# Performance work log

Measured on AMD Instinct MI355X. Metric: run time of the kernel, lower is better.

The kernel has to match this reference:

```python
import jax, jax.numpy as jnp
import numpy as np

N, M, D = 8192, 8192, 256

def setup_inputs() -> dict:
    key = jax.random.key(0)
    k1, k2, k3, k4 = jax.random.split(key, 4)
    x1 = jax.random.normal(k1, (N, D), dtype=jnp.float32)
    x2 = jax.random.normal(k2, (M, D), dtype=jnp.float32)
    alpha_raw = jax.random.normal(k3, (D,), dtype=jnp.float32)      # nn.Parameter(torch.randn(input_dim))
    variance_raw = jnp.ones((1,), dtype=jnp.float32)                # nn.Parameter(torch.ones(1))
    return {"x1": x1, "x2": x2, "alpha_raw": alpha_raw, "variance_raw": variance_raw}

def reference(x1, x2, alpha_raw, variance_raw):
    # alpha = softmax(alpha_raw^2), variance = variance_raw^2
    alpha = jax.nn.softmax(alpha_raw ** 2)                          # (D,)
    variance = variance_raw ** 2                                    # (1,)
    # GEMM rewrite of sum_d alpha_d (x1_i - x2_j)^2:
    #   ||x1*sqrt(a)||^2 - 2 (x1*sqrt(a))(x2*sqrt(a))^T + ||x2*sqrt(a)||^2
    sa = jnp.sqrt(alpha)
    a = x1 * sa                                                     # (N, D)
    b = x2 * sa                                                     # (M, D)
    sq = (jnp.sum(a * a, axis=-1)[:, None]
          - 2.0 * (a @ b.T)
          + jnp.sum(b * b, axis=-1)[None, :])                       # (N, M)
    sq = jnp.maximum(sq, 0.0)  # numerical guard; exact value is non-negative
    kernel = variance * jnp.exp(-0.5 * sq)                          # (N, M)
    if kernel.shape[0] == 1:
        kernel = jnp.squeeze(kernel)
    return kernel
```

## Files before the change

kernel.cpp:

```cpp
#include <hip/hip_runtime.h>
#include <stdint.h>

#define NROWS 8192
#define MCOLS 8192
#define KDIM  256

typedef __bf16 bf16x8 __attribute__((ext_vector_type(8)));
typedef float  floatx4 __attribute__((ext_vector_type(4)));

__device__ __forceinline__ unsigned short f32_to_bf16_rne(float f) {
    unsigned int u = __float_as_uint(f);
    u += 0x7FFFu + ((u >> 16) & 1u);
    return (unsigned short)(u >> 16);
}
__device__ __forceinline__ float bf16_to_f32(unsigned short h) {
    return __uint_as_float(((unsigned int)h) << 16);
}

__device__ __forceinline__ void async16(const void* g, void* l) {
    __builtin_amdgcn_global_load_lds(
        (const __attribute__((address_space(1))) unsigned int*)g,
        (__attribute__((address_space(3))) unsigned int*)l,
        16, 0, 0);
}

__global__ void prep_alpha(const float* __restrict__ araw, float* __restrict__ sa) {
    __shared__ float buf[256];
    int d = threadIdx.x;
    float z = araw[d];
    z = z * z;
    buf[d] = z;
    __syncthreads();
    for (int s = 128; s > 0; s >>= 1) {
        if (d < s) buf[d] = fmaxf(buf[d], buf[d + s]);
        __syncthreads();
    }
    float mx = buf[0];
    __syncthreads();
    float e = __expf(z - mx);
    buf[d] = e;
    __syncthreads();
    for (int s = 128; s > 0; s >>= 1) {
        if (d < s) buf[d] += buf[d + s];
        __syncthreads();
    }
    float sum = buf[0];
    sa[d] = sqrtf(e / sum);
}

__global__ void prep_rows(const float* __restrict__ x, const float* __restrict__ sa,
                          unsigned short* __restrict__ mat, float* __restrict__ rnorm) {
    __shared__ float buf[256];
    int row = blockIdx.x;
    int d = threadIdx.x;
    float v = x[(size_t)row * KDIM + d] * sa[d];
    unsigned short h = f32_to_bf16_rne(v);
    mat[(size_t)row * KDIM + d] = h;
    float fv = bf16_to_f32(h);
    buf[d] = fv * fv;
    __syncthreads();
    for (int s = 128; s > 0; s >>= 1) {
        if (d < s) buf[d] += buf[d + s];
        __syncthreads();
    }
    if (d == 0) rnorm[row] = buf[0];
}

__global__ __launch_bounds__(256) void rbf_gemm(
    const unsigned short* __restrict__ A, const unsigned short* __restrict__ B,
    const float* __restrict__ ra, const float* __restrict__ rb,
    const float* __restrict__ vraw, float* __restrict__ out)
{
    __shared__ unsigned short As[128 * 64];
    __shared__ unsigned short Bs[128 * 64];

    const int tid  = threadIdx.x;
    const int lane = tid & 63;
    const int wave = tid >> 6;
    const int bm = blockIdx.y;
    const int bn = blockIdx.x;
    const int wm = (wave & 1) * 64;
    const int wn = (wave >> 1) * 64;
    const int quad = lane >> 4;
    const int l15  = lane & 15;

    floatx4 acc[4][4];
#pragma unroll
    for (int i = 0; i < 4; i++)
#pragma unroll
        for (int j = 0; j < 4; j++) acc[i][j] = (floatx4)0.0f;

    for (int k0 = 0; k0 < KDIM; k0 += 64) {
#pragma unroll
        for (int it = 0; it < 4; ++it) {
            int c   = it * 256 + tid;
            int row = c >> 3;
            int kc  = c & 7;
            int gkc = kc ^ (row & 7);
            const unsigned short* gA = A + (size_t)(bm * 128 + row) * KDIM + k0 + gkc * 8;
            const unsigned short* gB = B + (size_t)(bn * 128 + row) * KDIM + k0 + gkc * 8;
            async16(gA, &As[c * 8]);
            async16(gB, &Bs[c * 8]);
        }
        __syncthreads();

#pragma unroll
        for (int ks = 0; ks < 2; ++ks) {
            bf16x8 af[4], bfr[4];
            int kc = ks * 4 + quad;
#pragma unroll
            for (int t = 0; t < 4; ++t) {
                int m  = wm + t * 16 + l15;
                int sa_ = m * 8 + (kc ^ (m & 7));
                af[t]  = *(const bf16x8*)&As[sa_ * 8];
                int n  = wn + t * 16 + l15;
                int sb_ = n * 8 + (kc ^ (n & 7));
                bfr[t] = *(const bf16x8*)&Bs[sb_ * 8];
            }
#pragma unroll
            for (int ti = 0; ti < 4; ++ti)
#pragma unroll
                for (int tj = 0; tj < 4; ++tj)
                    acc[ti][tj] = __builtin_amdgcn_mfma_f32_16x16x32_bf16(
                        af[ti], bfr[tj], acc[ti][tj], 0, 0, 0);
        }
        __syncthreads();
    }

    float variance = vraw[0] * vraw[0];
    float rbv[4];
#pragma unroll
    for (int tj = 0; tj < 4; ++tj) rbv[tj] = rb[bn * 128 + wn + tj * 16 + l15];
#pragma unroll
    for (int ti = 0; ti < 4; ++ti) {
        int rowbase = bm * 128 + wm + ti * 16 + quad * 4;
        float rav[4];
#pragma unroll
        for (int r = 0; r < 4; ++r) rav[r] = ra[rowbase + r];
#pragma unroll
        for (int tj = 0; tj < 4; ++tj) {
            int col = bn * 128 + wn + tj * 16 + l15;
#pragma unroll
            for (int r = 0; r < 4; ++r) {
                float s = rav[r] + rbv[tj] - 2.0f * acc[ti][tj][r];
                s = fmaxf(s, 0.0f);
                out[(size_t)(rowbase + r) * MCOLS + col] = variance * __expf(-0.5f * s);
            }
        }
    }
}

extern "C" void kernel_launch(void* const* d_in, const int* in_sizes, int n_in,
                              void* d_out, int out_size, void* d_ws, size_t ws_size,
                              hipStream_t stream) {
    const float* x1   = (const float*)d_in[0];
    const float* x2   = (const float*)d_in[1];
    const float* araw = (const float*)d_in[2];
    const float* vraw = (const float*)d_in[3];
    float* out = (float*)d_out;

    char* ws = (char*)d_ws;
    float* sa = (float*)ws;
    float* ra = (float*)(ws + 1024);
    float* rb = (float*)(ws + 1024 + 32768);
    unsigned short* Amat = (unsigned short*)(ws + 66560);
    unsigned short* Bmat = (unsigned short*)(ws + 66560 + (size_t)NROWS * KDIM * 2);

    prep_alpha<<<1, 256, 0, stream>>>(araw, sa);
    prep_rows<<<NROWS, 256, 0, stream>>>(x1, sa, Amat, ra);
    prep_rows<<<MCOLS, 256, 0, stream>>>(x2, sa, Bmat, rb);

    dim3 grid(MCOLS / 128, NROWS / 128);
    rbf_gemm<<<grid, 256, 0, stream>>>(Amat, Bmat, ra, rb, vraw, out);
}
```

Before: 311.1 us.

## Vectorize output stores via transposed MFMA, merge row prep, swizzle block order

Swaps the MFMA operand order so each lane holds four consecutive output columns. The epilogue can then write float4 nontemporal stores instead of scalar strided stores, with the distance algebra folded to -0.5 scaling and a fminf. The two row-prep launches are merged into one wave-per-row kernel that uses vector loads and a shuffle reduction, removing the shared-memory tree. GEMM blocks are remapped into groups of 8 row tiles for better L2 reuse of the A and B tiles.

```diff
diff --git a/kernel.cpp b/kernel.cpp
--- a/kernel.cpp
+++ b/kernel.cpp
@@ -48,22 +48,37 @@
     sa[d] = sqrtf(e / sum);
 }
 
-__global__ void prep_rows(const float* __restrict__ x, const float* __restrict__ sa,
-                          unsigned short* __restrict__ mat, float* __restrict__ rnorm) {
-    __shared__ float buf[256];
-    int row = blockIdx.x;
-    int d = threadIdx.x;
-    float v = x[(size_t)row * KDIM + d] * sa[d];
-    unsigned short h = f32_to_bf16_rne(v);
-    mat[(size_t)row * KDIM + d] = h;
-    float fv = bf16_to_f32(h);
-    buf[d] = fv * fv;
-    __syncthreads();
-    for (int s = 128; s > 0; s >>= 1) {
-        if (d < s) buf[d] += buf[d + s];
-        __syncthreads();
-    }
-    if (d == 0) rnorm[row] = buf[0];
+__global__ __launch_bounds__(256) void prep_rows_all(
+    const float* __restrict__ x1, const float* __restrict__ x2,
+    const float* __restrict__ sa,
+    unsigned short* __restrict__ Amat, unsigned short* __restrict__ Bmat,
+    float* __restrict__ ra, float* __restrict__ rb)
+{
+    int rg   = blockIdx.x * 4 + (threadIdx.x >> 6);
+    int lane = threadIdx.x & 63;
+
+    const float* x; unsigned short* mat; float* rn; int row;
+    if (rg < NROWS) { x = x1; mat = Amat; rn = ra; row = rg; }
+    else            { x = x2; mat = Bmat; rn = rb; row = rg - NROWS; }
+
+    float4 sv = ((const float4*)sa)[lane];
+    float4 xv = ((const float4*)(x + (size_t)row * KDIM))[lane];
+
+    unsigned short h0 = f32_to_bf16_rne(xv.x * sv.x);
+    unsigned short h1 = f32_to_bf16_rne(xv.y * sv.y);
+    unsigned short h2 = f32_to_bf16_rne(xv.z * sv.z);
+    unsigned short h3 = f32_to_bf16_rne(xv.w * sv.w);
+
+    ushort4 hv; hv.x = h0; hv.y = h1; hv.z = h2; hv.w = h3;
+    ((ushort4*)(mat + (size_t)row * KDIM))[lane] = hv;
+
+    float f0 = bf16_to_f32(h0), f1 = bf16_to_f32(h1),
+          f2 = bf16_to_f32(h2), f3 = bf16_to_f32(h3);
+    float nrm = f0 * f0 + f1 * f1 + f2 * f2 + f3 * f3;
+#pragma unroll
+    for (int off = 32; off > 0; off >>= 1)
+        nrm += __shfl_down(nrm, off, 64);
+    if (lane == 0) rn[row] = nrm;
 }
 
 __global__ __launch_bounds__(256) void rbf_gemm(
@@ -77,8 +92,13 @@
     const int tid  = threadIdx.x;
     const int lane = tid & 63;
     const int wave = tid >> 6;
-    const int bm = blockIdx.y;
-    const int bn = blockIdx.x;
+
+    const int lin = blockIdx.y * gridDim.x + blockIdx.x;
+    const int p   = lin >> 9;
+    const int w   = lin & 511;
+    const int bm  = (p << 3) + (w & 7);
+    const int bn  = w >> 3;
+
     const int wm = (wave & 1) * 64;
     const int wn = (wave >> 1) * 64;
     const int quad = lane >> 4;
@@ -122,30 +142,32 @@
 #pragma unroll
                 for (int tj = 0; tj < 4; ++tj)
                     acc[ti][tj] = __builtin_amdgcn_mfma_f32_16x16x32_bf16(
-                        af[ti], bfr[tj], acc[ti][tj], 0, 0, 0);
+                        bfr[tj], af[ti], acc[ti][tj], 0, 0, 0);
         }
         __syncthreads();
     }
 
     float variance = vraw[0] * vraw[0];
-    float rbv[4];
+    float hra[4];
 #pragma unroll
-    for (int tj = 0; tj < 4; ++tj) rbv[tj] = rb[bn * 128 + wn + tj * 16 + l15];
+    for (int ti = 0; ti < 4; ++ti)
+        hra[ti] = -0.5f * ra[bm * 128 + wm + ti * 16 + l15];
+
 #pragma unroll
-    for (int ti = 0; ti < 4; ++ti) {
-        int rowbase = bm * 128 + wm + ti * 16 + quad * 4;
-        float rav[4];
+    for (int tj = 0; tj < 4; ++tj) {
+        int jbase = bn * 128 + wn + tj * 16 + quad * 4;
+        float4 rb4 = *(const float4*)(rb + jbase);
+        float hrb0 = -0.5f * rb4.x, hrb1 = -0.5f * rb4.y,
+              hrb2 = -0.5f * rb4.z, hrb3 = -0.5f * rb4.w;
 #pragma unroll
-        for (int r = 0; r < 4; ++r) rav[r] = ra[rowbase + r];
-#pragma unroll
-        for (int tj = 0; tj < 4; ++tj) {
-            int col = bn * 128 + wn + tj * 16 + l15;
-#pragma unroll
-            for (int r = 0; r < 4; ++r) {
-                float s = rav[r] + rbv[tj] - 2.0f * acc[ti][tj][r];
-                s = fmaxf(s, 0.0f);
-                out[(size_t)(rowbase + r) * MCOLS + col] = variance * __expf(-0.5f * s);
-            }
+        for (int ti = 0; ti < 4; ++ti) {
+            int i = bm * 128 + wm + ti * 16 + l15;
+            floatx4 v;
+            v[0] = variance * __expf(fminf(acc[ti][tj][0] + hra[ti] + hrb0, 0.0f));
+            v[1] = variance * __expf(fminf(acc[ti][tj][1] + hra[ti] + hrb1, 0.0f));
+            v[2] = variance * __expf(fminf(acc[ti][tj][2] + hra[ti] + hrb2, 0.0f));
+            v[3] = variance * __expf(fminf(acc[ti][tj][3] + hra[ti] + hrb3, 0.0f));
+            __builtin_nontemporal_store(v, (floatx4*)(out + (size_t)i * MCOLS + jbase));
         }
     }
 }
@@ -167,8 +189,7 @@
     unsigned short* Bmat = (unsigned short*)(ws + 66560 + (size_t)NROWS * KDIM * 2);
 
     prep_alpha<<<1, 256, 0, stream>>>(araw, sa);
-    prep_rows<<<NROWS, 256, 0, stream>>>(x1, sa, Amat, ra);
-    prep_rows<<<MCOLS, 256, 0, stream>>>(x2, sa, Bmat, rb);
+    prep_rows_all<<<(NROWS + MCOLS) / 4, 256, 0, stream>>>(x1, x2, sa, Amat, Bmat, ra, rb);
 
     dim3 grid(MCOLS / 128, NROWS / 128);
     rbf_gemm<<<grid, 256, 0, stream>>>(Amat, Bmat, ra, rb, vraw, out);
```

Result: no change. 312.8 us (+0.5%).
